# Kernel tuning notes

Hardware: AMD Instinct MI355X
Metric: run time of the kernel (lower is better)

## Reference

```python
import jax, jax.numpy as jnp
import numpy as np

B, S, D, H = 2, 2048, 1024, 16
DK = D // H
ALPHA = 0.5


def setup_inputs() -> dict:
    key = jax.random.key(0)
    ks = jax.random.split(key, 16)
    scale = 0.02
    return {
        "q": jax.random.normal(ks[0], (B, S, D), dtype=jnp.float32),
        "k": jax.random.normal(ks[1], (B, S, D), dtype=jnp.float32),
        "v": jax.random.normal(ks[2], (B, S, D), dtype=jnp.float32),
        "attn_mask": jax.random.randint(ks[3], (S, S), 0, 2, dtype=jnp.int32),
        "causal_mask": jax.random.uniform(ks[4], (S, S), dtype=jnp.float32),
        "Wq": jax.random.normal(ks[5], (D, D), dtype=jnp.float32) * scale,
        "bq": jnp.zeros((D,), dtype=jnp.float32),
        "Wk": jax.random.normal(ks[6], (D, D), dtype=jnp.float32) * scale,
        "bk": jnp.zeros((D,), dtype=jnp.float32),
        "Wv": jax.random.normal(ks[7], (D, D), dtype=jnp.float32) * scale,
        "bv": jnp.zeros((D,), dtype=jnp.float32),
        "Wo": jax.random.normal(ks[8], (D, D), dtype=jnp.float32) * scale,
        "bo": jnp.zeros((D,), dtype=jnp.float32),
    }


def _split_heads(x):
    # [B, S, D] -> [B, H, S, DK]
    return x.reshape(B, S, H, DK).transpose(0, 2, 1, 3)


def reference(q, k, v, attn_mask, causal_mask, Wq, bq, Wk, bk, Wv, bv, Wo, bo):
    qh = _split_heads(q @ Wq.T + bq)
    kh = _split_heads(k @ Wk.T + bk)
    vh = _split_heads(v @ Wv.T + bv)
    scores = jnp.einsum("bhqd,bhkd->bhqk", qh, kh) / jnp.sqrt(jnp.float32(DK))
    # additive mask: positions where attn_mask == 1 get -1e9 (broadcast [S,S] -> [B,H,S,S])
    scores = jnp.where(attn_mask[None, None] == 1, jnp.float32(-1e9), scores)
    # multiplicative causal scaling (applied AFTER the fill, as in the original)
    scores = scores * (1.0 + ALPHA * causal_mask[None, None])
    probs = jax.nn.softmax(scores, axis=-1)  # dropout is identity in eval / p=0
    attn = jnp.einsum("bhqk,bhkd->bhqd", probs, vh)  # [B, H, S, DK]
    concat = attn.transpose(0, 2, 1, 3).reshape(B, S, D)
    out = concat @ Wo.T + bo
    return (out, attn)
```

## Files before the change

kernel.cpp:

```cpp
#include <hip/hip_runtime.h>
#include <hip/hip_bf16.h>

#define NB 2
#define NS 2048
#define ND 1024
#define NH 16
#define NDK 64
#define GK 1024

using bf16_t = __hip_bfloat16;
typedef __attribute__((ext_vector_type(8))) short bf16x8;
typedef __attribute__((ext_vector_type(4))) float f32x4;
typedef unsigned short u16;
typedef unsigned int u32;

#define SC_LOG2E 0.1803368801f

static __device__ __forceinline__ u16 f2bf(float f) {
    __hip_bfloat16 h = __float2bfloat16(f);
    return *reinterpret_cast<u16*>(&h);
}

static __device__ __forceinline__ u32 cvtpk2(float a, float b) {
    u32 r;
    asm("v_cvt_pk_bf16_f32 %0, %1, %2" : "=v"(r) : "v"(a), "v"(b));
    return r;
}

#define GLDS16(gp, lp)                                                                    \
    __builtin_amdgcn_global_load_lds((const __attribute__((address_space(1))) void*)(gp), \
                                     (__attribute__((address_space(3))) void*)(lp), 16, 0, 0)

struct PrepArgs {
    const float* qkv_s[3];
    u16* qkv_d[3];
    const float* w_s[4];
    u16* w_d[4];
    const int* am;
    const float* cm;
    float* comb;
};

__global__ __launch_bounds__(256) void prep_kernel(PrepArgs a) {
    const int x = blockIdx.x, y = blockIdx.y, tid = threadIdx.x;
    if (y < 3) {
        int i = x * 256 + tid;
        float4 v = reinterpret_cast<const float4*>(a.qkv_s[y])[i];
        ushort4 o;
        o.x = f2bf(v.x); o.y = f2bf(v.y); o.z = f2bf(v.z); o.w = f2bf(v.w);
        reinterpret_cast<ushort4*>(a.qkv_d[y])[i] = o;
    } else if (y == 3) {
        int w = x >> 10;
        int i = (x & 1023) * 256 + tid;
        float4 v = reinterpret_cast<const float4*>(a.w_s[w])[i];
        ushort4 o;
        o.x = f2bf(v.x); o.y = f2bf(v.y); o.z = f2bf(v.z); o.w = f2bf(v.w);
        reinterpret_cast<ushort4*>(a.w_d[w])[i] = o;
    } else {
        int i = (x * 256 + tid) * 4;
        int4 m = *reinterpret_cast<const int4*>(a.am + i);
        float4 c = *reinterpret_cast<const float4*>(a.cm + i);
        float4 r;
        r.x = (m.x == 1) ? -1.0f : fmaf(0.5f * SC_LOG2E, c.x, SC_LOG2E);
        r.y = (m.y == 1) ? -1.0f : fmaf(0.5f * SC_LOG2E, c.y, SC_LOG2E);
        r.z = (m.z == 1) ? -1.0f : fmaf(0.5f * SC_LOG2E, c.z, SC_LOG2E);
        r.w = (m.w == 1) ? -1.0f : fmaf(0.5f * SC_LOG2E, c.w, SC_LOG2E);
        *reinterpret_cast<float4*>(a.comb + i) = r;
    }
}

struct MMArgs {
    const u16* A;
    const u16* W;
    const float* bias;
    void* out;
    int mode;
};

template <int BN>
__global__ __launch_bounds__(256) void mm_glds(MMArgs g0, MMArgs g1, MMArgs g2) {
    const MMArgs ga = (blockIdx.z == 0) ? g0 : (blockIdx.z == 1) ? g1 : g2;
    constexpr int BM = 128, BK = 32;
    constexpr int JN = BN / 32;
    __shared__ __align__(16) u16 As[2][BM * BK];
    __shared__ __align__(16) u16 Bs[2][BN * BK];

    const int tid = threadIdx.x;
    const int lane = tid & 63;
    const int w = tid >> 6;
    const int wm = w >> 1, wn = w & 1;
    const int fr = lane & 15, fg = lane >> 4;
    const int bm0 = blockIdx.y * BM, bn0 = blockIdx.x * BN;

    const u16* agp = ga.A + (size_t)(bm0 + w * 32 + (lane >> 2)) * GK + (lane & 3) * 8;
    const u16* bgp = ga.W +
                     (size_t)(bn0 + w * (BN == 128 ? 32 : 16) + (lane >> 2)) * GK +
                     (lane & 3) * 8;

    f32x4 acc[4][JN];
    const f32x4 z4 = {0.f, 0.f, 0.f, 0.f};
#pragma unroll
    for (int i = 0; i < 4; ++i)
#pragma unroll
        for (int j = 0; j < JN; ++j) acc[i][j] = z4;

    {
        u16* la = &As[0][w * 1024];
        u16* lb = &Bs[0][w * (BN == 128 ? 1024 : 512)];
        GLDS16(agp, la);
        GLDS16(agp + 16 * GK, la + 512);
        if (BN == 128) {
            GLDS16(bgp, lb);
            GLDS16(bgp + 16 * GK, lb + 512);
        } else {
            GLDS16(bgp, lb);
        }
    }
    __syncthreads();

    int cur = 0;
    for (int kt = 0; kt < GK / BK; ++kt) {
        if (kt + 1 < GK / BK) {
            const int ko = (kt + 1) * BK;
            u16* la = &As[cur ^ 1][w * 1024];
            u16* lb = &Bs[cur ^ 1][w * (BN == 128 ? 1024 : 512)];
            GLDS16(agp + ko, la);
            GLDS16(agp + ko + 16 * GK, la + 512);
            if (BN == 128) {
                GLDS16(bgp + ko, lb);
                GLDS16(bgp + ko + 16 * GK, lb + 512);
            } else {
                GLDS16(bgp + ko, lb);
            }
        }
        bf16x8 af[4], bfr[JN];
#pragma unroll
        for (int i = 0; i < 4; ++i)
            af[i] = *(const bf16x8*)&As[cur][(wm * 64 + i * 16 + fr) * BK + fg * 8];
#pragma unroll
        for (int j = 0; j < JN; ++j)
            bfr[j] = *(const bf16x8*)&Bs[cur][(wn * (BN / 2) + j * 16 + fr) * BK + fg * 8];
#pragma unroll
        for (int i = 0; i < 4; ++i)
#pragma unroll
            for (int j = 0; j < JN; ++j)
                acc[i][j] = __builtin_amdgcn_mfma_f32_16x16x32_bf16(af[i], bfr[j], acc[i][j],
                                                                    0, 0, 0);
        __syncthreads();
        cur ^= 1;
    }

#pragma unroll
    for (int j = 0; j < JN; ++j) {
        const int col = bn0 + wn * (BN / 2) + j * 16 + fr;
        const float bv_ = ga.bias[col];
        if (ga.mode == 2) {
            const int h_ = col >> 6, dk = col & (NDK - 1);
#pragma unroll
            for (int i = 0; i < 4; ++i) {
                const int row0 = bm0 + wm * 64 + i * 16 + fg * 4;
                const int b_ = row0 >> 11, s_ = row0 & (NS - 1);
                uint2 pw;
                pw.x = cvtpk2(acc[i][j][0] + bv_, acc[i][j][1] + bv_);
                pw.y = cvtpk2(acc[i][j][2] + bv_, acc[i][j][3] + bv_);
                *(uint2*)((u16*)ga.out +
                          (((size_t)(b_ * NH + h_)) * NDK + dk) * NS + s_) = pw;
            }
        } else {
#pragma unroll
            for (int i = 0; i < 4; ++i) {
#pragma unroll
                for (int r = 0; r < 4; ++r) {
                    const int row = bm0 + wm * 64 + i * 16 + fg * 4 + r;
                    const float val = acc[i][j][r] + bv_;
                    if (ga.mode == 1) {
                        const int b_ = row >> 11, s_ = row & (NS - 1);
                        const int h_ = col >> 6, dk = col & (NDK - 1);
                        ((bf16_t*)ga.out)[(((size_t)(b_ * NH + h_)) * NS + s_) * NDK + dk] =
                            __float2bfloat16(val);
                    } else {
                        ((float*)ga.out)[(size_t)row * ND + col] = val;
                    }
                }
            }
        }
    }
}

__global__ __launch_bounds__(256) void flash_mfma(const u16* __restrict__ Qh,
                                                  const u16* __restrict__ Kh,
                                                  const u16* __restrict__ VhT,
                                                  const float* __restrict__ comb,
                                                  float* __restrict__ attnOut,
                                                  u16* __restrict__ concatOut) {
    __shared__ __align__(16) char smem[40960];

    const int tid = threadIdx.x;
    const int w = tid >> 6;
    const int lane = tid & 63;
    const int qc = lane & 15;
    const int g = lane >> 4;
    const int bh = blockIdx.y;
    const int b_ = bh >> 4, h_ = bh & 15;
    const int qw = blockIdx.x * 64 + w * 16;

    const size_t bhoff = (size_t)bh * NS * NDK;

    const u32 kxl = qc & 3;
    const u32 kx2 = (qc >> 2) & 1;

    const int srow = lane >> 3;
    const int sblk = (lane & 7) ^ srow;
    const u16* kgp = Kh + bhoff + (size_t)(w * 16 + srow) * NDK + sblk * 8;
    const u16* vgp = VhT + bhoff + (size_t)(w * 16 + srow) * NS + sblk * 8;
    char* kdst = smem + w * 2048;
    char* vdst = smem + 16384 + w * 2048;

    bf16x8 qf0, qf1;
    {
        const u16* qp = Qh + bhoff + (size_t)(qw + qc) * NDK + g * 8;
        qf0 = *(const bf16x8*)(qp);
        qf1 = *(const bf16x8*)(qp + 32);
    }

    bf16x8 vones;
#pragma unroll
    for (int j = 0; j < 8; ++j) vones[j] = (short)0x3F80;

    const f32x4 z4 = {0.f, 0.f, 0.f, 0.f};
    f32x4 o[4];
    o[0] = o[1] = o[2] = o[3] = z4;
    f32x4 o_l = z4;

    const u32 cA = kx2 << 6;
    const u32 cB = cA ^ 64;
    const u32 laneRC = (u32)qc * 128 + ((g ^ kxl) << 4);
    const char* kb0 = smem + laneRC + cA;
    const char* kb1 = smem + laneRC + cB;
    const char* vb0 = smem + 16384 + laneRC + cA;
    const char* vb1 = smem + 16384 + laneRC + cB;
    char* ptrow = smem + 32768 + w * 2048 + qc * 128;
    const char* prd0 = ptrow + ((g ^ kxl) << 4) + cA;
    const char* prd1 = ptrow + ((g ^ kxl) << 4) + cB;
    char* pwb = ptrow + (u32)((g * 8) ^ ((qc & 1) << 4));
    const u32 sxb = (u32)((qc >> 1) & 3) << 5;

    const float* cbp = comb + (size_t)(qw + qc) * NS + g * 4;

    GLDS16(kgp, kdst);
    GLDS16(kgp + 8 * NDK, kdst + 1024);
    GLDS16(vgp, vdst);
    GLDS16(vgp + 8 * NS, vdst + 1024);
    const u16* kgn = kgp + 64 * NDK;
    const u16* vgn = vgp + 64;
    __syncthreads();

    u32 koff = 0;
    for (int kt = 0; kt < NS; kt += 64) {
        if (kt + 64 < NS) {
            char* kd = kdst + (koff ^ 8192);
            char* vd = vdst + (koff ^ 8192);
            GLDS16(kgn, kd);
            GLDS16(kgn + 8 * NDK, kd + 1024);
            GLDS16(vgn, vd);
            GLDS16(vgn + 8 * NS, vd + 1024);
            kgn += 64 * NDK;
            vgn += 64;
        }

        f32x4 s[4];
        s[0] = s[1] = s[2] = s[3] = z4;
#pragma unroll
        for (int ks = 0; ks < 4; ++ks) {
            bf16x8 kf0 = *(const bf16x8*)(kb0 + koff + ks * 2048);
            bf16x8 kf1 = *(const bf16x8*)(kb1 + koff + ks * 2048);
            s[ks] = __builtin_amdgcn_mfma_f32_16x16x32_bf16(kf0, qf0, s[ks], 0, 0, 0);
            s[ks] = __builtin_amdgcn_mfma_f32_16x16x32_bf16(kf1, qf1, s[ks], 0, 0, 0);
        }

#pragma unroll
        for (int ks = 0; ks < 4; ++ks) {
            float4 c4 = *(const float4*)(cbp + ks * 16);
            const float* cc = (const float*)&c4;
            float p0 = __builtin_amdgcn_exp2f(s[ks][0] * cc[0]);
            float p1 = __builtin_amdgcn_exp2f(s[ks][1] * cc[1]);
            float p2 = __builtin_amdgcn_exp2f(s[ks][2] * cc[2]);
            float p3 = __builtin_amdgcn_exp2f(s[ks][3] * cc[3]);
            p0 = (cc[0] < 0.f) ? 0.f : p0;
            p1 = (cc[1] < 0.f) ? 0.f : p1;
            p2 = (cc[2] < 0.f) ? 0.f : p2;
            p3 = (cc[3] < 0.f) ? 0.f : p3;
            uint2 pw;
            pw.x = cvtpk2(p0, p1);
            pw.y = cvtpk2(p2, p3);
            *(uint2*)(pwb + (((u32)(ks * 32)) ^ sxb)) = pw;
        }
        cbp += 64;

        asm volatile("s_waitcnt lgkmcnt(0)" ::: "memory");
        __builtin_amdgcn_sched_barrier(0);

        bf16x8 pf0 = *(const bf16x8*)(prd0);
        bf16x8 pf1 = *(const bf16x8*)(prd1);
        o_l = __builtin_amdgcn_mfma_f32_16x16x32_bf16(pf0, vones, o_l, 0, 0, 0);
        o_l = __builtin_amdgcn_mfma_f32_16x16x32_bf16(pf1, vones, o_l, 0, 0, 0);
#pragma unroll
        for (int dsub = 0; dsub < 4; ++dsub) {
            bf16x8 vf0 = *(const bf16x8*)(vb0 + koff + dsub * 2048);
            bf16x8 vf1 = *(const bf16x8*)(vb1 + koff + dsub * 2048);
            o[dsub] = __builtin_amdgcn_mfma_f32_16x16x32_bf16(pf0, vf0, o[dsub], 0, 0, 0);
            o[dsub] = __builtin_amdgcn_mfma_f32_16x16x32_bf16(pf1, vf1, o[dsub], 0, 0, 0);
        }
        __syncthreads();
        koff ^= 8192;
    }

    float inv[4];
#pragma unroll
    for (int r = 0; r < 4; ++r) inv[r] = 1.0f / o_l[r];

#pragma unroll
    for (int dsub = 0; dsub < 4; ++dsub) {
#pragma unroll
        for (int r = 0; r < 4; ++r) {
            const float val = o[dsub][r] * inv[r];
            const int qg = qw + g * 4 + r;
            const int d = dsub * 16 + qc;
            attnOut[bhoff + (size_t)qg * NDK + d] = val;
            concatOut[((size_t)b_ * NS + qg) * ND + h_ * NDK + d] = f2bf(val);
        }
    }
}

extern "C" void kernel_launch(void* const* d_in, const int* in_sizes, int n_in,
                              void* d_out, int out_size, void* d_ws, size_t ws_size,
                              hipStream_t stream) {
    const float* q = (const float*)d_in[0];
    const float* k = (const float*)d_in[1];
    const float* v = (const float*)d_in[2];
    const int* am = (const int*)d_in[3];
    const float* cm = (const float*)d_in[4];
    const float* Wq = (const float*)d_in[5];
    const float* bq = (const float*)d_in[6];
    const float* Wk = (const float*)d_in[7];
    const float* bk = (const float*)d_in[8];
    const float* Wv = (const float*)d_in[9];
    const float* bv = (const float*)d_in[10];
    const float* Wo = (const float*)d_in[11];
    const float* bo = (const float*)d_in[12];

    float* out = (float*)d_out;
    float* attn_out = out + (size_t)NB * NS * ND;

    char* p = (char*)d_ws;
    float* CB = (float*)p;  p += (size_t)NS * NS * 4;
    u16* qb = (u16*)p;      p += (size_t)NB * NS * ND * 2;
    u16* kb_ = (u16*)p;     p += (size_t)NB * NS * ND * 2;
    u16* vb_ = (u16*)p;     p += (size_t)NB * NS * ND * 2;
    u16* Wqb = (u16*)p;     p += (size_t)ND * ND * 2;
    u16* Wkb = (u16*)p;     p += (size_t)ND * ND * 2;
    u16* Wvb = (u16*)p;     p += (size_t)ND * ND * 2;
    u16* Wob = (u16*)p;     p += (size_t)ND * ND * 2;
    u16* Qh = (u16*)p;      p += (size_t)NB * NS * ND * 2;
    u16* Kh = (u16*)p;      p += (size_t)NB * NS * ND * 2;
    u16* VhT = (u16*)p;     p += (size_t)NB * NS * ND * 2;
    u16* CCb = (u16*)p;     p += (size_t)NB * NS * ND * 2;

    PrepArgs pa;
    pa.qkv_s[0] = q;  pa.qkv_d[0] = qb;
    pa.qkv_s[1] = k;  pa.qkv_d[1] = kb_;
    pa.qkv_s[2] = v;  pa.qkv_d[2] = vb_;
    pa.w_s[0] = Wq;   pa.w_d[0] = Wqb;
    pa.w_s[1] = Wk;   pa.w_d[1] = Wkb;
    pa.w_s[2] = Wv;   pa.w_d[2] = Wvb;
    pa.w_s[3] = Wo;   pa.w_d[3] = Wob;
    pa.am = am;
    pa.cm = cm;
    pa.comb = CB;
    hipLaunchKernelGGL(prep_kernel, dim3(4096, 5), dim3(256), 0, stream, pa);

    MMArgs mq = {qb, Wqb, bq, (void*)Qh, 1};
    MMArgs mk = {kb_, Wkb, bk, (void*)Kh, 1};
    MMArgs mv = {vb_, Wvb, bv, (void*)VhT, 2};
    hipLaunchKernelGGL((mm_glds<128>), dim3(ND / 128, 4096 / 128, 3), dim3(256), 0, stream,
                       mq, mk, mv);

    hipLaunchKernelGGL(flash_mfma, dim3(NS / 64, NB * NH), dim3(256), 0, stream, Qh, Kh, VhT,
                       CB, attn_out, CCb);

    MMArgs mo = {CCb, Wob, bo, (void*)out, 0};
    hipLaunchKernelGGL((mm_glds<64>), dim3(ND / 64, 4096 / 128, 1), dim3(256), 0, stream,
                       mo, mo, mo);
}
```

Before: 171.3 us.

## Stage K/V tiles through registers with two-deep prefetch instead of direct LDS loads

Replaces the direct global-to-LDS async copies with plain global loads into registers, issued two tiles ahead. The staged data is written into the alternate LDS buffer after the softmax step of each iteration. The loop is unrolled by two so the register sets alternate, and __syncthreads is replaced by raw s_barrier calls. The aim is to hide global load latency behind more compute, at the cost of extra VGPRs for staging. The last iterations also issue loads past the end of each head's K/V slice.

```diff
diff --git a/kernel.cpp b/kernel.cpp
--- a/kernel.cpp
+++ b/kernel.cpp
@@ -211,10 +211,11 @@
 
     const int srow = lane >> 3;
     const int sblk = (lane & 7) ^ srow;
-    const u16* kgp = Kh + bhoff + (size_t)(w * 16 + srow) * NDK + sblk * 8;
-    const u16* vgp = VhT + bhoff + (size_t)(w * 16 + srow) * NS + sblk * 8;
-    char* kdst = smem + w * 2048;
-    char* vdst = smem + 16384 + w * 2048;
+    const u16* kgn = Kh + bhoff + (size_t)(w * 16 + srow) * NDK + sblk * 8;
+    const u16* vgn = VhT + bhoff + (size_t)(w * 16 + srow) * NS + sblk * 8;
+
+    char* kwrA = smem + w * 2048 + lane * 16;
+    char* vwrA = kwrA + 16384;
 
     bf16x8 qf0, qf1;
     {
@@ -247,73 +248,82 @@
 
     const float* cbp = comb + (size_t)(qw + qc) * NS + g * 4;
 
-    GLDS16(kgp, kdst);
-    GLDS16(kgp + 8 * NDK, kdst + 1024);
-    GLDS16(vgp, vdst);
-    GLDS16(vgp + 8 * NS, vdst + 1024);
-    const u16* kgn = kgp + 64 * NDK;
-    const u16* vgn = vgp + 64;
-    __syncthreads();
-
-    u32 koff = 0;
-    for (int kt = 0; kt < NS; kt += 64) {
-        if (kt + 64 < NS) {
-            char* kd = kdst + (koff ^ 8192);
-            char* vd = vdst + (koff ^ 8192);
-            GLDS16(kgn, kd);
-            GLDS16(kgn + 8 * NDK, kd + 1024);
-            GLDS16(vgn, vd);
-            GLDS16(vgn + 8 * NS, vd + 1024);
-            kgn += 64 * NDK;
-            vgn += 64;
-        }
-
-        f32x4 s[4];
-        s[0] = s[1] = s[2] = s[3] = z4;
-#pragma unroll
-        for (int ks = 0; ks < 4; ++ks) {
-            bf16x8 kf0 = *(const bf16x8*)(kb0 + koff + ks * 2048);
-            bf16x8 kf1 = *(const bf16x8*)(kb1 + koff + ks * 2048);
-            s[ks] = __builtin_amdgcn_mfma_f32_16x16x32_bf16(kf0, qf0, s[ks], 0, 0, 0);
-            s[ks] = __builtin_amdgcn_mfma_f32_16x16x32_bf16(kf1, qf1, s[ks], 0, 0, 0);
-        }
-
-#pragma unroll
-        for (int ks = 0; ks < 4; ++ks) {
-            float4 c4 = *(const float4*)(cbp + ks * 16);
-            const float* cc = (const float*)&c4;
-            float p0 = __builtin_amdgcn_exp2f(s[ks][0] * cc[0]);
-            float p1 = __builtin_amdgcn_exp2f(s[ks][1] * cc[1]);
-            float p2 = __builtin_amdgcn_exp2f(s[ks][2] * cc[2]);
-            float p3 = __builtin_amdgcn_exp2f(s[ks][3] * cc[3]);
-            p0 = (cc[0] < 0.f) ? 0.f : p0;
-            p1 = (cc[1] < 0.f) ? 0.f : p1;
-            p2 = (cc[2] < 0.f) ? 0.f : p2;
-            p3 = (cc[3] < 0.f) ? 0.f : p3;
-            uint2 pw;
-            pw.x = cvtpk2(p0, p1);
-            pw.y = cvtpk2(p2, p3);
-            *(uint2*)(pwb + (((u32)(ks * 32)) ^ sxb)) = pw;
-        }
-        cbp += 64;
-
-        asm volatile("s_waitcnt lgkmcnt(0)" ::: "memory");
-        __builtin_amdgcn_sched_barrier(0);
-
-        bf16x8 pf0 = *(const bf16x8*)(prd0);
-        bf16x8 pf1 = *(const bf16x8*)(prd1);
-        o_l = __builtin_amdgcn_mfma_f32_16x16x32_bf16(pf0, vones, o_l, 0, 0, 0);
-        o_l = __builtin_amdgcn_mfma_f32_16x16x32_bf16(pf1, vones, o_l, 0, 0, 0);
-#pragma unroll
-        for (int dsub = 0; dsub < 4; ++dsub) {
-            bf16x8 vf0 = *(const bf16x8*)(vb0 + koff + dsub * 2048);
-            bf16x8 vf1 = *(const bf16x8*)(vb1 + koff + dsub * 2048);
-            o[dsub] = __builtin_amdgcn_mfma_f32_16x16x32_bf16(pf0, vf0, o[dsub], 0, 0, 0);
-            o[dsub] = __builtin_amdgcn_mfma_f32_16x16x32_bf16(pf1, vf1, o[dsub], 0, 0, 0);
-        }
-        __syncthreads();
-        koff ^= 8192;
-    }
+    int4 kaA, kbA, vaA, vbA;
+    int4 kaB, kbB, vaB, vbB;
+
+#define FL_LDG(KA, KB, VA, VB)                          \
+    KA = *(const int4*)(kgn);                           \
+    KB = *(const int4*)(kgn + 8 * NDK);                 \
+    VA = *(const int4*)(vgn);                           \
+    VB = *(const int4*)(vgn + 8 * NS);                  \
+    kgn += 64 * NDK;                                    \
+    vgn += 64;
+
+    FL_LDG(kaA, kbA, vaA, vbA)
+    FL_LDG(kaB, kbB, vaB, vbB)
+    *(int4*)(kwrA) = kaA;
+    *(int4*)(kwrA + 1024) = kbA;
+    *(int4*)(vwrA) = vaA;
+    *(int4*)(vwrA + 1024) = vbA;
+    asm volatile("s_waitcnt lgkmcnt(0)" ::: "memory");
+    __builtin_amdgcn_s_barrier();
+    asm volatile("" ::: "memory");
+
+#define FL_PHASE(KOFF, LKA, LKB, LVA, LVB, WKA, WKB, WVA, WVB)                            \
+    {                                                                                     \
+        FL_LDG(LKA, LKB, LVA, LVB)                                                        \
+        f32x4 s[4];                                                                       \
+        s[0] = s[1] = s[2] = s[3] = z4;                                                   \
+        _Pragma("unroll") for (int ks = 0; ks < 4; ++ks) {                                \
+            bf16x8 kf0 = *(const bf16x8*)(kb0 + (KOFF) + ks * 2048);                      \
+            bf16x8 kf1 = *(const bf16x8*)(kb1 + (KOFF) + ks * 2048);                      \
+            s[ks] = __builtin_amdgcn_mfma_f32_16x16x32_bf16(kf0, qf0, s[ks], 0, 0, 0);    \
+            s[ks] = __builtin_amdgcn_mfma_f32_16x16x32_bf16(kf1, qf1, s[ks], 0, 0, 0);    \
+        }                                                                                 \
+        _Pragma("unroll") for (int ks = 0; ks < 4; ++ks) {                                \
+            float4 c4 = *(const float4*)(cbp + ks * 16);                                  \
+            const float* cc = (const float*)&c4;                                          \
+            float p0 = __builtin_amdgcn_exp2f(s[ks][0] * cc[0]);                          \
+            float p1 = __builtin_amdgcn_exp2f(s[ks][1] * cc[1]);                          \
+            float p2 = __builtin_amdgcn_exp2f(s[ks][2] * cc[2]);                          \
+            float p3 = __builtin_amdgcn_exp2f(s[ks][3] * cc[3]);                          \
+            p0 = (cc[0] < 0.f) ? 0.f : p0;                                                \
+            p1 = (cc[1] < 0.f) ? 0.f : p1;                                                \
+            p2 = (cc[2] < 0.f) ? 0.f : p2;                                                \
+            p3 = (cc[3] < 0.f) ? 0.f : p3;                                                \
+            uint2 pw;                                                                     \
+            pw.x = cvtpk2(p0, p1);                                                        \
+            pw.y = cvtpk2(p2, p3);                                                        \
+            *(uint2*)(pwb + (((u32)(ks * 32)) ^ sxb)) = pw;                               \
+        }                                                                                 \
+        cbp += 64;                                                                        \
+        *(int4*)(kwrA + ((KOFF) ^ 8192)) = WKA;                                           \
+        *(int4*)(kwrA + ((KOFF) ^ 8192) + 1024) = WKB;                                    \
+        *(int4*)(vwrA + ((KOFF) ^ 8192)) = WVA;                                           \
+        *(int4*)(vwrA + ((KOFF) ^ 8192) + 1024) = WVB;                                    \
+        asm volatile("s_waitcnt lgkmcnt(0)" ::: "memory");                                \
+        __builtin_amdgcn_sched_barrier(0);                                                \
+        bf16x8 pf0 = *(const bf16x8*)(prd0);                                              \
+        bf16x8 pf1 = *(const bf16x8*)(prd1);                                              \
+        o_l = __builtin_amdgcn_mfma_f32_16x16x32_bf16(pf0, vones, o_l, 0, 0, 0);          \
+        o_l = __builtin_amdgcn_mfma_f32_16x16x32_bf16(pf1, vones, o_l, 0, 0, 0);          \
+        _Pragma("unroll") for (int dsub = 0; dsub < 4; ++dsub) {                          \
+            bf16x8 vf0 = *(const bf16x8*)(vb0 + (KOFF) + dsub * 2048);                    \
+            bf16x8 vf1 = *(const bf16x8*)(vb1 + (KOFF) + dsub * 2048);                    \
+            o[dsub] = __builtin_amdgcn_mfma_f32_16x16x32_bf16(pf0, vf0, o[dsub], 0, 0, 0);\
+            o[dsub] = __builtin_amdgcn_mfma_f32_16x16x32_bf16(pf1, vf1, o[dsub], 0, 0, 0);\
+        }                                                                                 \
+        asm volatile("" ::: "memory");                                                    \
+        __builtin_amdgcn_s_barrier();                                                     \
+        asm volatile("" ::: "memory");                                                    \
+    }
+
+    for (int it = 0; it < 16; ++it) {
+        FL_PHASE(0, kaA, kbA, vaA, vbA, kaB, kbB, vaB, vbB)
+        FL_PHASE(8192, kaB, kbB, vaB, vbB, kaA, kbA, vaA, vbA)
+    }
+#undef FL_PHASE
+#undef FL_LDG
 
     float inv[4];
 #pragma unroll
```

After: 198.1 us. 1.16x slower.
